# Kernel optimization log

Measured on AMD Instinct MI355X. Metric: run time of the kernel, lower is better.

## Reference

```python
import jax, jax.numpy as jnp
import numpy as np
from jax import lax

ROUTING_ITERS = 3
EPS = 1e-8


def _conv(x, w, b, stride=1):
    # x: [B,C,H,W], w: [O,C,kh,kw]  (VALID padding, NCHW/OIHW)
    y = lax.conv_general_dilated(x, w, (stride, stride), 'VALID',
                                 dimension_numbers=('NCHW', 'OIHW', 'NCHW'))
    return y + b[None, :, None, None]


def _maxpool2(x):
    return lax.reduce_window(x, -jnp.inf, lax.max, (1, 1, 2, 2), (1, 1, 2, 2), 'VALID')


def _squash(s, axis=-1):
    n2 = jnp.sum(s * s, axis=axis, keepdims=True)
    return s * (n2 / (1.0 + n2)) / jnp.sqrt(n2 + EPS)


def setup_inputs() -> dict:
    key = jax.random.key(0)
    ks = jax.random.split(key, 9)
    p = lambda k, shp: (jax.random.normal(k, shp, dtype=jnp.float32) * 0.05)
    return {
        'x':  jax.random.normal(ks[0], (64, 1, 92, 92), dtype=jnp.float32),
        'w1': p(ks[1], (128, 1, 9, 9)),   'b1': jnp.zeros((128,), jnp.float32),
        'w2': p(ks[2], (64, 128, 5, 5)),  'b2': jnp.zeros((64,), jnp.float32),
        'wc': p(ks[3], (128, 64, 8, 8)),  'bc': jnp.zeros((128,), jnp.float32),
        # routing transform: [num_primary=1024, num_sar=10, out_dim=16, in_dim=32]
        'Wr': p(ks[4], (1024, 10, 16, 32)),
    }


def reference(x, w1, b1, w2, b2, wc, bc, Wr):
    B = x.shape[0]
    # feature extractor (dropout is identity at inference)
    h = jax.nn.relu(_conv(x, w1, b1))          # [B,128,84,84]
    h = _maxpool2(h)                            # [B,128,42,42]
    h = _conv(h, w2, b2)                        # [B,64,38,38]
    # primary capsule conv
    h = _conv(h, wc, bc, stride=2)              # [B,128,16,16]
    # 128 channels = 4 capsule types * 32-dim capsules, 16x16 spatial -> 1024 caps
    u = h.reshape(B, 4, 32, 16, 16).transpose(0, 1, 3, 4, 2).reshape(B, 1024, 32)
    u = _squash(u)                              # [B,1024,32]
    # u_hat: predictions of each primary cap for each SAR cap
    u_hat = jnp.einsum('bpi,ptoi->bpto', u, Wr)  # [B,1024,10,16]
    # dynamic routing
    b_log = jnp.zeros((B, 1024, 10), dtype=x.dtype)
    for _ in range(ROUTING_ITERS):
        c = jax.nn.softmax(b_log, axis=2)               # [B,1024,10]
        s = jnp.einsum('bpt,bpto->bto', c, u_hat)       # [B,10,16]
        v = _squash(s)                                   # [B,10,16]
        b_log = b_log + jnp.einsum('bpto,bto->bpt', u_hat, v)
    likelihood = jnp.sqrt(jnp.sum(v * v, axis=-1) + EPS)  # [B,10]
    return likelihood
```

## Files before the change

kernel.cpp:

```cpp
#include <hip/hip_runtime.h>
#include <hip/hip_bf16.h>
#include <math.h>


#define EPSF 1e-8f

typedef __bf16 bf16x8 __attribute__((ext_vector_type(8)));
typedef __bf16 bf16x4 __attribute__((ext_vector_type(4)));
typedef float floatx4 __attribute__((ext_vector_type(4)));
typedef float floatx16 __attribute__((ext_vector_type(16)));

__global__ __launch_bounds__(256) void k_t_w1b(const float* __restrict__ w1, __bf16* __restrict__ w1b) {
    int i = blockIdx.x * 256 + threadIdx.x;
    if (i >= 12288) return;
    int kt = i >> 10, oc = (i >> 3) & 127, j = i & 7;
    int k = kt * 8 + j;
    w1b[i] = (__bf16)(k < 81 ? w1[oc * 81 + k] : 0.f);
}

__global__ __launch_bounds__(256) void k_t_w2a(const float* __restrict__ w2, __bf16* __restrict__ w2a) {
    int i = blockIdx.x * 256 + threadIdx.x;
    if (i >= 204800) return;
    int j = i & 7, lane = (i >> 3) & 63, f = i >> 9;
    int mt = f & 1, ks = (f >> 1) & 3, rem = f >> 3;
    int khw = rem % 25, icc = rem / 25;
    int c32 = lane & 31, h = lane >> 5;
    int oc = mt * 32 + c32;
    int ic = icc * 64 + ks * 16 + h * 8 + j;
    w2a[i] = (__bf16)w2[(oc * 128 + ic) * 25 + khw];
}

__global__ __launch_bounds__(256) void k_t_wca(const float* __restrict__ wc, __bf16* __restrict__ wca) {
    int i = blockIdx.x * 256 + threadIdx.x;
    if (i >= 524288) return;
    int j = i & 7, lane = (i >> 3) & 63, f = i >> 9;
    int ct = f & 3, ks = (f >> 2) & 1, khw = (f >> 3) & 63, icc = f >> 9;
    int c32 = lane & 31, h = lane >> 5;
    int oc = ct * 32 + c32;
    int ic = icc * 32 + ks * 16 + h * 8 + j;
    wca[i] = (__bf16)wc[(oc * 64 + ic) * 64 + khw];
}

__global__ __launch_bounds__(256) void k_t_wrb(const float* __restrict__ Wr, __bf16* __restrict__ wrb) {
    int i = blockIdx.x * 256 + threadIdx.x;
    if (i >= 5242880) return;
    wrb[i] = (__bf16)Wr[i];
}

__global__ __launch_bounds__(256, 3) void k_conv1_mfma(const float* __restrict__ x,
                                                       const __bf16* __restrict__ w1b,
                                                       const float* __restrict__ b1,
                                                       __bf16* __restrict__ h1n) {
    __shared__ float xs[960];
    __shared__ __bf16 Bl[18432];
    int py = blockIdx.x, ocg = blockIdx.y, b = blockIdx.z;
    int t = threadIdx.x;
    int lane = t & 63, w = t >> 6;
    int cc = lane & 15, q = lane >> 4;

    const float* xb = x + (size_t)b * 8464 + 2 * py * 92;
    for (int j = t; j < 920; j += 256) xs[j] = xb[j];

    int ocA = ocg * 64 + w * 16 + cc;
    bf16x8 af[3];
#pragma unroll
    for (int ks = 0; ks < 3; ++ks)
        af[ks] = *(const bf16x8*)(w1b + ((ks * 4 + q) * 128 + ocA) * 8);

    __syncthreads();

    if (t < 192) {
        int row = t / 96, pos = t - (t / 96) * 96;
        int sbase = row * 92 + pos;
        bool pvalid = pos < 84;
#pragma unroll
        for (int kt = 0; kt < 12; ++kt) {
            bf16x8 pk;
#pragma unroll
            for (int j = 0; j < 8; ++j) {
                int k = kt * 8 + j;
                int kh = k / 9, kw = k - kh * 9;
                float v = (pvalid && k < 81) ? xs[sbase + kh * 92 + kw] : 0.f;
                pk[j] = (__bf16)v;
            }
            *(bf16x8*)(Bl + ((kt * 2 + row) * 96 + pos) * 8) = pk;
        }
    }
    __syncthreads();

    floatx4 acc[2][6];
    const char* Bb = (const char*)Bl + cc * 16 + q * 3072;
#pragma unroll
    for (int rr = 0; rr < 2; ++rr)
#pragma unroll
        for (int n6 = 0; n6 < 6; ++n6) {
            floatx4 a = (floatx4){0.f, 0.f, 0.f, 0.f};
#pragma unroll
            for (int ks = 0; ks < 3; ++ks) {
                bf16x8 bf = *(const bf16x8*)(Bb + ks * 12288 + rr * 1536 + n6 * 256);
                a = __builtin_amdgcn_mfma_f32_16x16x32_bf16(af[ks], bf, a, 0, 0, 0);
            }
            acc[rr][n6] = a;
        }

    int oc0 = ocg * 64 + w * 16 + q * 4;
    float4 bv = *(const float4*)(b1 + oc0);
    size_t obase = (((size_t)b * 42 + py) * 42) * 128 + oc0;
#pragma unroll
    for (int n6 = 0; n6 < 6; ++n6) {
        bf16x4 pk;
#pragma unroll
        for (int r = 0; r < 4; ++r) {
            float vert = fmaxf(acc[0][n6][r], acc[1][n6][r]);
            float hz = fmaxf(vert, __shfl_xor(vert, 1, 64));
            float pooled = fmaxf(hz + ((const float*)&bv)[r], 0.f);
            pk[r] = (__bf16)pooled;
        }
        if ((cc & 1) == 0) {
            int px = n6 * 8 + (cc >> 1);
            if (px < 42)
                *(bf16x4*)(h1n + obase + (size_t)px * 128) = pk;
        }
    }
}

__global__ __launch_bounds__(256, 2) void k_conv2(const __bf16* __restrict__ h1n,
                                                  const __bf16* __restrict__ w2a,
                                                  float* __restrict__ p01) {
    __shared__ __bf16 ins[25704];
    int g = blockIdx.x, b = blockIdx.y, icc = blockIdx.z;
    int row0 = g * 5;
    int t = threadIdx.x;
    int lane = t & 63, w = t >> 6;
    int c32 = lane & 31, h = lane >> 5;
    int validp = (g < 7) ? 190 : 114;
    int ic0 = icc * 64;

    int baseN[2], posi[2];
#pragma unroll
    for (int nt = 0; nt < 2; ++nt) {
        int pi = (w * 2 + nt) * 32 + c32;
        int pc = pi < validp ? pi : validp - 1;
        int r = pc / 38, c = pc - r * 38;
        posi[nt] = pi;
        baseN[nt] = (r * 42 + c) * 136 + h * 16;
    }

#pragma unroll
    for (int half = 0; half < 2; ++half) {
        uint4 rb[6];
        int lo[6];
#pragma unroll
        for (int k = 0; k < 6; ++k) {
            int j = (half * 6 + k) * 256 + t;
            if (j > 3023) j -= 256;
            int lr = j / 336, rem = j - lr * 336;
            int ix = rem >> 3, sb = rem & 7;
            int rg = row0 + lr; if (rg > 41) rg = 41;
            rb[k] = *(const uint4*)(h1n + ((((size_t)b * 42 + rg) * 42 + ix) * 128 + ic0 + sb * 8));
            lo[k] = (lr * 42 + ix) * 136 + sb * 16;
        }
#pragma unroll
        for (int k = 0; k < 6; ++k)
            *(uint4*)((char*)ins + lo[k]) = rb[k];
    }

    floatx16 acc[2][2];
#pragma unroll
    for (int mt = 0; mt < 2; ++mt)
#pragma unroll
        for (int nt = 0; nt < 2; ++nt)
#pragma unroll
            for (int i = 0; i < 16; ++i) acc[mt][nt][i] = 0.f;

    __syncthreads();
    const __bf16* wic = w2a + (size_t)icc * 25 * 4096 + (lane << 3);
#pragma unroll
    for (int khw = 0; khw < 25; ++khw) {
        int kh = khw / 5, kw = khw - kh * 5;
        int doff = (kh * 42 + kw) * 136;
        const __bf16* wk = wic + khw * 4096;
#pragma unroll
        for (int ks = 0; ks < 4; ++ks) {
            bf16x8 a0 = *(const bf16x8*)(wk + ks * 1024);
            bf16x8 a1 = *(const bf16x8*)(wk + ks * 1024 + 512);
#pragma unroll
            for (int nt = 0; nt < 2; ++nt) {
                bf16x8 bfr = *(const bf16x8*)((char*)ins + baseN[nt] + doff + ks * 32);
                acc[0][nt] = __builtin_amdgcn_mfma_f32_32x32x16_bf16(a0, bfr, acc[0][nt], 0, 0, 0);
                acc[1][nt] = __builtin_amdgcn_mfma_f32_32x32x16_bf16(a1, bfr, acc[1][nt], 0, 0, 0);
            }
        }
    }
    float* pdst = p01 + (size_t)icc * 5914624;
#pragma unroll
    for (int nt = 0; nt < 2; ++nt) {
        int pi = posi[nt];
        if (pi < validp) {
            int r = pi / 38, c = pi - r * 38;
            int oh = row0 + r;
            size_t obase = (((size_t)b * 38 + oh) * 38 + c) * 64;
#pragma unroll
            for (int mt = 0; mt < 2; ++mt) {
#pragma unroll
                for (int g2 = 0; g2 < 4; ++g2) {
                    int oc0 = mt * 32 + g2 * 8 + h * 4;
                    floatx4 pv;
                    pv[0] = acc[mt][nt][g2 * 4 + 0];
                    pv[1] = acc[mt][nt][g2 * 4 + 1];
                    pv[2] = acc[mt][nt][g2 * 4 + 2];
                    pv[3] = acc[mt][nt][g2 * 4 + 3];
                    *(floatx4*)(pdst + obase + oc0) = pv;
                }
            }
        }
    }
}

__global__ __launch_bounds__(256) void k_reduce_h2(const float* __restrict__ p01,
                                                   const float* __restrict__ b2,
                                                   __bf16* __restrict__ h2n) {
    int i = blockIdx.x * 256 + threadIdx.x;
    if (i >= 1478656) return;
    size_t e = (size_t)i * 4;
    floatx4 a = *(const floatx4*)(p01 + e);
    floatx4 b = *(const floatx4*)(p01 + 5914624 + e);
    floatx4 bv = *(const floatx4*)(b2 + ((i * 4) & 63));
    bf16x4 pk;
    pk.x = (__bf16)(a[0] + b[0] + bv[0]);
    pk.y = (__bf16)(a[1] + b[1] + bv[1]);
    pk.z = (__bf16)(a[2] + b[2] + bv[2]);
    pk.w = (__bf16)(a[3] + b[3] + bv[3]);
    *(bf16x4*)(h2n + e) = pk;
}

__global__ __launch_bounds__(256, 4) void k_convcaps(const __bf16* __restrict__ h2n,
                                                     const __bf16* __restrict__ wca,
                                                     const float* __restrict__ bc,
                                                     __bf16* __restrict__ ub) {
    __shared__ __bf16 ins[13680];
    int g = blockIdx.x, b = blockIdx.y;
    int t = threadIdx.x;
    int lane = t & 63, ct = t >> 6;
    int c32 = lane & 31, h = lane >> 5;
    int rloc = c32 >> 4, cx = c32 & 15;

    floatx16 acc;
#pragma unroll
    for (int i = 0; i < 16; ++i) acc[i] = 0.f;

    int Bbase = (76 * rloc + cx) * 72 + h * 16;
    for (int icc = 0; icc < 2; ++icc) {
        int ic0 = icc * 32;
        __syncthreads();
        {
            uint4 rb[6];
            int lo[6];
#pragma unroll
            for (int k = 0; k < 6; ++k) {
                int j = k * 256 + t;
                if (j > 1519) j -= 256;
                int r = j / 152, rem = j - r * 152;
                int c = rem >> 2, s = rem & 3;
                rb[k] = *(const uint4*)(h2n + ((((size_t)b * 38 + 4 * g + r) * 38 + c) * 64 + ic0 + s * 8));
                int X = (r * 2 + (c & 1)) * 19 + (c >> 1);
                lo[k] = X * 72 + s * 16;
            }
#pragma unroll
            for (int k = 0; k < 6; ++k)
                *(uint4*)((char*)ins + lo[k]) = rb[k];
        }
        __syncthreads();
        const __bf16* wic = wca + ((size_t)icc * 64 * 8 + ct) * 512 + (lane << 3);
#pragma unroll
        for (int khw = 0; khw < 64; ++khw) {
            int kh = khw >> 3, kw = khw & 7;
            int par = kw & 1, k2 = kw >> 1;
            int doff = ((kh * 2 + par) * 19 + k2) * 72;
            const __bf16* wk = wic + khw * 4096;
#pragma unroll
            for (int ks = 0; ks < 2; ++ks) {
                bf16x8 af = *(const bf16x8*)(wk + ks * 2048);
                bf16x8 bfr = *(const bf16x8*)((char*)ins + Bbase + doff + ks * 32);
                acc = __builtin_amdgcn_mfma_f32_32x32x16_bf16(af, bfr, acc, 0, 0, 0);
            }
        }
    }
    float vals[16];
    float n2p = 0.f;
#pragma unroll
    for (int g2 = 0; g2 < 4; ++g2) {
        float4 bv = *(const float4*)(bc + ct * 32 + g2 * 8 + h * 4);
#pragma unroll
        for (int j = 0; j < 4; ++j) {
            float v = acc[g2 * 4 + j] + ((const float*)&bv)[j];
            vals[g2 * 4 + j] = v;
            n2p = fmaf(v, v, n2p);
        }
    }
    float n2 = n2p + __shfl_xor(n2p, 32, 64);
    float scale = (n2 / (1.f + n2)) / sqrtf(n2 + EPSF);
    int pos = (2 * g + rloc) * 16 + cx;
    __bf16* dst = ub + (((size_t)b * 1024 + ct * 256 + pos) * 32);
#pragma unroll
    for (int g2 = 0; g2 < 4; ++g2) {
        bf16x4 pk;
        pk.x = (__bf16)(vals[g2 * 4 + 0] * scale);
        pk.y = (__bf16)(vals[g2 * 4 + 1] * scale);
        pk.z = (__bf16)(vals[g2 * 4 + 2] * scale);
        pk.w = (__bf16)(vals[g2 * 4 + 3] * scale);
        *(bf16x4*)(dst + g2 * 8 + h * 4) = pk;
    }
}

__global__ __launch_bounds__(256, 2) void k_uhat(const __bf16* __restrict__ ub,
                                                 const __bf16* __restrict__ wrb,
                                                 __bf16* __restrict__ uhT) {
    int pt = blockIdx.x, ts = blockIdx.y, bz = blockIdx.z;
    int t = threadIdx.x;
    int p = pt * 64 + (t & 63);
    int q = t >> 6;
    bf16x8 wf[4][4];
#pragma unroll
    for (int o4 = 0; o4 < 4; ++o4)
#pragma unroll
        for (int j = 0; j < 4; ++j)
            wf[o4][j] = *(const bf16x8*)(wrb + (((size_t)p * 10 + ts) * 16 + q * 4 + o4) * 32 + j * 8);
#pragma unroll 1
    for (int bi = 0; bi < 16; ++bi) {
        int b = bz * 16 + bi;
        bf16x8 uf[4];
        const bf16x8* up = (const bf16x8*)(ub + ((size_t)b * 1024 + p) * 32);
#pragma unroll
        for (int j = 0; j < 4; ++j) uf[j] = up[j];
#pragma unroll
        for (int o4 = 0; o4 < 4; ++o4) {
            float s = 0.f;
#pragma unroll
            for (int j = 0; j < 4; ++j)
#pragma unroll
                for (int e = 0; e < 8; ++e)
                    s = fmaf((float)uf[j][e], (float)wf[o4][j][e], s);
            uhT[(((size_t)b * 10 + ts) * 16 + q * 4 + o4) * 1024 + p] = (__bf16)s;
        }
    }
}

__global__ __launch_bounds__(256) void k_route(const __bf16* __restrict__ uhT,
                                               const float* __restrict__ blR,
                                               float* __restrict__ blW,
                                               float* __restrict__ out,
                                               int first, int dob, int last) {
    __shared__ __bf16 uh_s[16384];
    __shared__ float sred[4][16];
    __shared__ float vs[16];
    int b = blockIdx.x, tt = blockIdx.y;
    int t = threadIdx.x;
    const __bf16* uhb = uhT + ((size_t)b * 10 + tt) * 16384;
#pragma unroll
    for (int k = 0; k < 8; ++k) {
        int j = k * 256 + t;
        *(uint4*)((char*)uh_s + j * 16) = *(const uint4*)((const char*)uhb + j * 16);
    }
    __syncthreads();

    float acc[16];
#pragma unroll
    for (int o = 0; o < 16; ++o) acc[o] = 0.f;
    const float* blb = blR + b * 10240;
    for (int p = t; p < 1024; p += 256) {
        float c;
        if (first) {
            c = 0.1f;
        } else {
            float den = 0.f, et = 0.f;
#pragma unroll
            for (int tp = 0; tp < 10; ++tp) {
                float e = expf(blb[tp * 1024 + p]);
                den += e;
                if (tp == tt) et = e;
            }
            c = et / den;
        }
#pragma unroll
        for (int o = 0; o < 16; ++o)
            acc[o] = fmaf(c, (float)uh_s[o * 1024 + p], acc[o]);
    }
    int lane = t & 63, wid = t >> 6;
#pragma unroll
    for (int o = 0; o < 16; ++o) {
        float v = acc[o];
#pragma unroll
        for (int off = 32; off >= 1; off >>= 1) v += __shfl_xor(v, off, 64);
        if (lane == 0) sred[wid][o] = v;
    }
    __syncthreads();
    if (t < 16) {
        float s = (sred[0][t] + sred[1][t]) + (sred[2][t] + sred[3][t]);
        float n2 = s * s;
#pragma unroll
        for (int off = 1; off < 16; off <<= 1) n2 += __shfl_xor(n2, off, 16);
        float scale = (n2 / (1.f + n2)) / sqrtf(n2 + EPSF);
        vs[t] = s * scale;
        if (last && t == 0) {
            float sv2 = n2 * scale * scale;
            out[b * 10 + tt] = sqrtf(sv2 + EPSF);
        }
    }
    __syncthreads();

    if (dob) {
        const float* blr = blR + (b * 10 + tt) * 1024;
        float* blw = blW + (b * 10 + tt) * 1024;
        for (int p = t; p < 1024; p += 256) {
            float d = 0.f;
#pragma unroll
            for (int o = 0; o < 16; ++o) d = fmaf((float)uh_s[o * 1024 + p], vs[o], d);
            blw[p] = first ? d : (blr[p] + d);
        }
    }
}

extern "C" void kernel_launch(void* const* d_in, const int* in_sizes, int n_in,
                              void* d_out, int out_size, void* d_ws, size_t ws_size,
                              hipStream_t stream) {
    const float* x  = (const float*)d_in[0];
    const float* w1 = (const float*)d_in[1];
    const float* b1 = (const float*)d_in[2];
    const float* w2 = (const float*)d_in[3];
    const float* b2 = (const float*)d_in[4];
    const float* wc = (const float*)d_in[5];
    const float* bc = (const float*)d_in[6];
    const float* Wr = (const float*)d_in[7];
    float* out = (float*)d_out;
    float* ws  = (float*)d_ws;

    __bf16* w2a = (__bf16*)(ws);
    __bf16* wca = (__bf16*)(ws + 102400);
    __bf16* w1b = (__bf16*)(ws + 364544);
    __bf16* h1n = (__bf16*)(ws + 375040);
    __bf16* h2n = (__bf16*)(ws + 7600384);
    __bf16* ub  = (__bf16*)(ws + 12654848);
    float*  blA = ws + 14752000;
    __bf16* wrb = (__bf16*)(ws + 15417600);
    float*  p01 = ws + 18039040;
    float*  blB = ws + 29868288;
    __bf16* uhT = (__bf16*)(ws + 375040);

    k_t_w1b<<<48, 256, 0, stream>>>(w1, w1b);
    k_t_w2a<<<800, 256, 0, stream>>>(w2, w2a);
    k_t_wca<<<2048, 256, 0, stream>>>(wc, wca);
    k_t_wrb<<<20480, 256, 0, stream>>>(Wr, wrb);
    k_conv1_mfma<<<dim3(42, 2, 64), 256, 0, stream>>>(x, w1b, b1, h1n);
    k_conv2<<<dim3(8, 64, 2), 256, 0, stream>>>(h1n, w2a, p01);
    k_reduce_h2<<<5776, 256, 0, stream>>>(p01, b2, h2n);
    k_convcaps<<<dim3(8, 64), 256, 0, stream>>>(h2n, wca, bc, ub);
    k_uhat<<<dim3(16, 10, 4), 256, 0, stream>>>(ub, wrb, uhT);
    k_route<<<dim3(64, 10), 256, 0, stream>>>(uhT, blA, blA, out, 1, 1, 0);
    k_route<<<dim3(64, 10), 256, 0, stream>>>(uhT, blA, blB, out, 0, 1, 0);
    k_route<<<dim3(64, 10), 256, 0, stream>>>(uhT, blB, blB, out, 0, 0, 1);
}
```

Baseline: 314.8 us.

## Merge weight-conversion kernels and prefetch conv2 weights two taps ahead

Folds the four weight-conversion kernels into a single launch covering all index ranges, which removes three kernel launches and their tail gaps. In conv2, the A-fragment weight loads are held in a three-slot register ring and issued two taps ahead of the MFMAs that consume them, so global load latency can overlap with compute. The occupancy hint of 2 blocks per CU is dropped from conv2's launch bounds to leave room for the extra registers the ring needs. The risk is higher register pressure and lower occupancy in conv2.

```diff
diff --git a/kernel.cpp b/kernel.cpp
--- a/kernel.cpp
+++ b/kernel.cpp
@@ -10,41 +10,46 @@
 typedef float floatx4 __attribute__((ext_vector_type(4)));
 typedef float floatx16 __attribute__((ext_vector_type(16)));
 
-__global__ __launch_bounds__(256) void k_t_w1b(const float* __restrict__ w1, __bf16* __restrict__ w1b) {
+__global__ __launch_bounds__(256) void k_t_all(const float* __restrict__ Wr,
+                                               const float* __restrict__ wc,
+                                               const float* __restrict__ w2,
+                                               const float* __restrict__ w1,
+                                               __bf16* __restrict__ wrb,
+                                               __bf16* __restrict__ wca,
+                                               __bf16* __restrict__ w2a,
+                                               __bf16* __restrict__ w1b) {
     int i = blockIdx.x * 256 + threadIdx.x;
-    if (i >= 12288) return;
-    int kt = i >> 10, oc = (i >> 3) & 127, j = i & 7;
-    int k = kt * 8 + j;
-    w1b[i] = (__bf16)(k < 81 ? w1[oc * 81 + k] : 0.f);
-}
-
-__global__ __launch_bounds__(256) void k_t_w2a(const float* __restrict__ w2, __bf16* __restrict__ w2a) {
-    int i = blockIdx.x * 256 + threadIdx.x;
-    if (i >= 204800) return;
-    int j = i & 7, lane = (i >> 3) & 63, f = i >> 9;
-    int mt = f & 1, ks = (f >> 1) & 3, rem = f >> 3;
-    int khw = rem % 25, icc = rem / 25;
-    int c32 = lane & 31, h = lane >> 5;
-    int oc = mt * 32 + c32;
-    int ic = icc * 64 + ks * 16 + h * 8 + j;
-    w2a[i] = (__bf16)w2[(oc * 128 + ic) * 25 + khw];
-}
-
-__global__ __launch_bounds__(256) void k_t_wca(const float* __restrict__ wc, __bf16* __restrict__ wca) {
-    int i = blockIdx.x * 256 + threadIdx.x;
-    if (i >= 524288) return;
-    int j = i & 7, lane = (i >> 3) & 63, f = i >> 9;
-    int ct = f & 3, ks = (f >> 2) & 1, khw = (f >> 3) & 63, icc = f >> 9;
-    int c32 = lane & 31, h = lane >> 5;
-    int oc = ct * 32 + c32;
-    int ic = icc * 32 + ks * 16 + h * 8 + j;
-    wca[i] = (__bf16)wc[(oc * 64 + ic) * 64 + khw];
-}
-
-__global__ __launch_bounds__(256) void k_t_wrb(const float* __restrict__ Wr, __bf16* __restrict__ wrb) {
-    int i = blockIdx.x * 256 + threadIdx.x;
-    if (i >= 5242880) return;
-    wrb[i] = (__bf16)Wr[i];
+    if (i < 5242880) {
+        wrb[i] = (__bf16)Wr[i];
+        return;
+    }
+    int i2 = i - 5242880;
+    if (i2 < 524288) {
+        int j = i2 & 7, lane = (i2 >> 3) & 63, f = i2 >> 9;
+        int ct = f & 3, ks = (f >> 2) & 1, khw = (f >> 3) & 63, icc = f >> 9;
+        int c32 = lane & 31, h = lane >> 5;
+        int oc = ct * 32 + c32;
+        int ic = icc * 32 + ks * 16 + h * 8 + j;
+        wca[i2] = (__bf16)wc[(oc * 64 + ic) * 64 + khw];
+        return;
+    }
+    int i3 = i2 - 524288;
+    if (i3 < 204800) {
+        int j = i3 & 7, lane = (i3 >> 3) & 63, f = i3 >> 9;
+        int mt = f & 1, ks = (f >> 1) & 3, rem = f >> 3;
+        int khw = rem % 25, icc = rem / 25;
+        int c32 = lane & 31, h = lane >> 5;
+        int oc = mt * 32 + c32;
+        int ic = icc * 64 + ks * 16 + h * 8 + j;
+        w2a[i3] = (__bf16)w2[(oc * 128 + ic) * 25 + khw];
+        return;
+    }
+    int i4 = i3 - 204800;
+    if (i4 < 12288) {
+        int kt = i4 >> 10, oc = (i4 >> 3) & 127, j = i4 & 7;
+        int k = kt * 8 + j;
+        w1b[i4] = (__bf16)(k < 81 ? w1[oc * 81 + k] : 0.f);
+    }
 }
 
 __global__ __launch_bounds__(256, 3) void k_conv1_mfma(const float* __restrict__ x,
@@ -124,9 +129,9 @@
     }
 }
 
-__global__ __launch_bounds__(256, 2) void k_conv2(const __bf16* __restrict__ h1n,
-                                                  const __bf16* __restrict__ w2a,
-                                                  float* __restrict__ p01) {
+__global__ __launch_bounds__(256) void k_conv2(const __bf16* __restrict__ h1n,
+                                               const __bf16* __restrict__ w2a,
+                                               float* __restrict__ p01) {
     __shared__ __bf16 ins[25704];
     int g = blockIdx.x, b = blockIdx.y, icc = blockIdx.z;
     int row0 = g * 5;
@@ -173,17 +178,34 @@
 #pragma unroll
             for (int i = 0; i < 16; ++i) acc[mt][nt][i] = 0.f;
 
-    __syncthreads();
     const __bf16* wic = w2a + (size_t)icc * 25 * 4096 + (lane << 3);
+
+    bf16x8 abuf[3][8];
+#pragma unroll
+    for (int ks = 0; ks < 4; ++ks) {
+        abuf[0][ks * 2]     = *(const bf16x8*)(wic + 0 * 4096 + ks * 1024);
+        abuf[0][ks * 2 + 1] = *(const bf16x8*)(wic + 0 * 4096 + ks * 1024 + 512);
+        abuf[1][ks * 2]     = *(const bf16x8*)(wic + 1 * 4096 + ks * 1024);
+        abuf[1][ks * 2 + 1] = *(const bf16x8*)(wic + 1 * 4096 + ks * 1024 + 512);
+    }
+
+    __syncthreads();
 #pragma unroll
     for (int khw = 0; khw < 25; ++khw) {
+        if (khw + 2 < 25) {
+            const __bf16* wk2 = wic + (khw + 2) * 4096;
+#pragma unroll
+            for (int ks = 0; ks < 4; ++ks) {
+                abuf[(khw + 2) % 3][ks * 2]     = *(const bf16x8*)(wk2 + ks * 1024);
+                abuf[(khw + 2) % 3][ks * 2 + 1] = *(const bf16x8*)(wk2 + ks * 1024 + 512);
+            }
+        }
         int kh = khw / 5, kw = khw - kh * 5;
         int doff = (kh * 42 + kw) * 136;
-        const __bf16* wk = wic + khw * 4096;
 #pragma unroll
         for (int ks = 0; ks < 4; ++ks) {
-            bf16x8 a0 = *(const bf16x8*)(wk + ks * 1024);
-            bf16x8 a1 = *(const bf16x8*)(wk + ks * 1024 + 512);
+            bf16x8 a0 = abuf[khw % 3][ks * 2];
+            bf16x8 a1 = abuf[khw % 3][ks * 2 + 1];
 #pragma unroll
             for (int nt = 0; nt < 2; ++nt) {
                 bf16x8 bfr = *(const bf16x8*)((char*)ins + baseN[nt] + doff + ks * 32);
@@ -447,10 +469,7 @@
     float*  blB = ws + 29868288;
     __bf16* uhT = (__bf16*)(ws + 375040);
 
-    k_t_w1b<<<48, 256, 0, stream>>>(w1, w1b);
-    k_t_w2a<<<800, 256, 0, stream>>>(w2, w2a);
-    k_t_wca<<<2048, 256, 0, stream>>>(wc, wca);
-    k_t_wrb<<<20480, 256, 0, stream>>>(Wr, wrb);
+    k_t_all<<<23376, 256, 0, stream>>>(Wr, wc, w2, w1, wrb, wca, w2a, w1b);
     k_conv1_mfma<<<dim3(42, 2, 64), 256, 0, stream>>>(x, w1b, b1, h1n);
     k_conv2<<<dim3(8, 64, 2), 256, 0, stream>>>(h1n, w2a, p01);
     k_reduce_h2<<<5776, 256, 0, stream>>>(p01, b2, h2n);
```

Measured after the change: 307.1 us. 2.4% less time.
